# Kernel tuning notes

Hardware: AMD Instinct MI355X
Metric: run time of the kernel (lower is better)

## Reference

```python
import jax, jax.numpy as jnp
import numpy as np

IN_CH, OUT_CH, K, STRIDE, PAD, NUM_POINTS = 16, 32, 3, 1, 1, 3
NUM_INPUTS = IN_CH * K * K  # 144
BATCH, H, W = 8, 32, 32


def setup_inputs() -> dict:
    key = jax.random.key(0)
    k1, k2, k3 = jax.random.split(key, 3)
    x = jax.random.normal(k1, (BATCH, IN_CH, H, W), dtype=jnp.float32)
    # sorted breakpoint positions per (input, output) pair in [-1, 1]
    base = jnp.linspace(-1.0, 1.0, NUM_POINTS, dtype=jnp.float32)
    jitter = 0.2 * (jax.random.uniform(k2, (NUM_INPUTS, OUT_CH, NUM_POINTS), dtype=jnp.float32) - 0.5) / NUM_POINTS
    positions = jnp.sort(base[None, None, :] + jitter, axis=-1)  # (I, O, P), sorted
    values = 0.1 * jax.random.normal(k3, (NUM_INPUTS, OUT_CH, NUM_POINTS), dtype=jnp.float32)
    return {"x": x, "positions": positions, "values": values}


def _gather_pt(table, idx):
    # table: (I, O, P), idx: (N, I, O) -> (N, I, O)
    return jnp.take_along_axis(table[None], idx[..., None], axis=-1)[..., 0]


def _piecewise(patches, positions, values):
    # patches: (N, I); positions/values: (I, O, P)
    P = positions.shape[-1]
    # bucket index: number of breakpoints <= x, clipped to a valid segment
    cmp = patches[:, :, None, None] >= positions[None]       # (N, I, O, P)
    idx = jnp.clip(cmp.sum(axis=-1) - 1, 0, P - 2)           # (N, I, O)
    pl = _gather_pt(positions, idx)
    pr = _gather_pt(positions, idx + 1)
    vl = _gather_pt(values, idx)
    vr = _gather_pt(values, idx + 1)
    t = (patches[:, :, None] - pl) / (pr - pl)               # (N, I, O)
    y = vl + t * (vr - vl)                                   # per-pair piecewise-linear value
    return y.sum(axis=1)                                     # (N, O): sum over input dims


def reference(x, positions, values):
    B, C, Hi, Wi = x.shape
    Ho = (Hi + 2 * PAD - K) // STRIDE + 1
    Wo = (Wi + 2 * PAD - K) // STRIDE + 1
    # im2col / unfold: (B, C*K*K, Ho, Wo) with (c, kh, kw) feature ordering like torch unfold
    patches = jax.lax.conv_general_dilated_patches(
        x, (K, K), (STRIDE, STRIDE), ((PAD, PAD), (PAD, PAD)))
    patches = patches.reshape(B, NUM_INPUTS, Ho * Wo).transpose(0, 2, 1).reshape(-1, NUM_INPUTS)
    out = _piecewise(patches, positions, values)             # (B*Ho*Wo, O)
    out = out.reshape(B, Ho * Wo, OUT_CH).transpose(0, 2, 1)
    return out.reshape(B, OUT_CH, Ho, Wo)
```

## Files before the change

kernel.cpp:

```cpp
#include <hip/hip_runtime.h>

#define IN_CH 16
#define OUT_CH 32
#define NUM_INPUTS 144
#define H_ 32
#define W_ 32
#define TILE_H 8
#define LDS_H 10
#define LDS_W 34
#define CSPLIT 8
#define TAPS (CSPLIT*9)

typedef __attribute__((ext_vector_type(2))) float f32x2;

__global__ void apc_prep(const float* __restrict__ pos,
                         const float* __restrict__ val,
                         float* __restrict__ tabP, float* __restrict__ tabM,
                         float* __restrict__ tabD, float* __restrict__ tabB) {
    int e = blockIdx.x * 256 + threadIdx.x;
    const float* pp = pos + e * 3;
    const float* vv = val + e * 3;
    float p0 = pp[0], p1 = pp[1], p2 = pp[2];
    float v0 = vv[0], v1 = vv[1], v2 = vv[2];
    float m0 = (v1 - v0) / (p1 - p0);
    float m1 = (v2 - v1) / (p2 - p1);
    tabP[e] = p1;
    tabM[e] = m0;
    tabD[e] = m1 - m0;
    tabB[e] = v0 - m0 * p0;
}

__global__ __launch_bounds__(256, 2) void apc_main(
        const float* __restrict__ x,
        const f32x2* __restrict__ tabP, const f32x2* __restrict__ tabM,
        const f32x2* __restrict__ tabD, const f32x2* __restrict__ tabB,
        float* __restrict__ out) {
    __shared__ float lx[CSPLIT * LDS_H * LDS_W];
    __shared__ f32x2 b0s[2];

    int bx  = blockIdx.x;
    int b   = bx >> 2;
    int ho0 = (bx & 3) * TILE_H;
    int pr0 = blockIdx.y * 2;
    int c0  = blockIdx.z * CSPLIT;
    int tid = threadIdx.x;
    int i0  = c0 * 9;

    for (int idx = tid; idx < CSPLIT * LDS_H * LDS_W; idx += 256) {
        int c   = idx / (LDS_H * LDS_W);
        int rem = idx - c * (LDS_H * LDS_W);
        int r   = rem / LDS_W;
        int col = rem - r * LDS_W;
        int gr  = ho0 + r - 1;
        int gc  = col - 1;
        float v = 0.f;
        if ((unsigned)gr < (unsigned)H_ && (unsigned)gc < (unsigned)W_)
            v = x[((b * IN_CH + c0 + c) * H_ + gr) * W_ + gc];
        lx[idx] = v;
    }

    int wave = tid >> 6, lane = tid & 63;
    if (wave < 2) {
        f32x2 s = {0.f, 0.f};
        for (int t = lane; t < TAPS; t += 64)
            s += tabB[(i0 + t) * 16 + pr0 + wave];
        #pragma unroll
        for (int off = 32; off; off >>= 1) {
            s.x += __shfl_down(s.x, off);
            s.y += __shfl_down(s.y, off);
        }
        if (lane == 0) b0s[wave] = s;
    }
    __syncthreads();

    int rl    = tid >> 5;
    int col   = tid & 31;
    int baseA = rl * LDS_W + col;

    f32x2 a0 = {0.f, 0.f}, h0 = {0.f, 0.f};
    f32x2 a1 = {0.f, 0.f}, h1 = {0.f, 0.f};
    const f32x2 zz = {0.f, 0.f};

    #pragma unroll
    for (int c = 0; c < CSPLIT; ++c) {
        #pragma unroll
        for (int kh = 0; kh < 3; ++kh) {
            #pragma unroll
            for (int kw = 0; kw < 3; ++kw) {
                int t  = (c * 3 + kh) * 3 + kw;
                int ti = (i0 + t) * 16;
                float p = lx[c * (LDS_H * LDS_W) + kh * LDS_W + kw + baseA];
                f32x2 pb = {p, p};
                f32x2 P0 = tabP[ti + pr0], P1 = tabP[ti + pr0 + 1];
                f32x2 M0 = tabM[ti + pr0], M1 = tabM[ti + pr0 + 1];
                f32x2 D0 = tabD[ti + pr0], D1 = tabD[ti + pr0 + 1];
                f32x2 r0 = __builtin_elementwise_max(pb - P0, zz);
                f32x2 r1 = __builtin_elementwise_max(pb - P1, zz);
                a0 = __builtin_elementwise_fma(M0, pb, a0);
                a1 = __builtin_elementwise_fma(M1, pb, a1);
                h0 = __builtin_elementwise_fma(D0, r0, h0);
                h1 = __builtin_elementwise_fma(D1, r1, h1);
            }
        }
    }

    a0 += h0 + b0s[0];
    a1 += h1 + b0s[1];

    int ho = ho0 + rl;
    int o0 = pr0 * 2;
    int ob = ((b * OUT_CH + o0) * H_ + ho) * W_ + col;
    atomicAdd(&out[ob            ], a0.x);
    atomicAdd(&out[ob +     H_*W_], a0.y);
    atomicAdd(&out[ob + 2 * H_*W_], a1.x);
    atomicAdd(&out[ob + 3 * H_*W_], a1.y);
}

extern "C" void kernel_launch(void* const* d_in, const int* in_sizes, int n_in,
                              void* d_out, int out_size, void* d_ws, size_t ws_size,
                              hipStream_t stream) {
    const float* x   = (const float*)d_in[0];
    const float* pos = (const float*)d_in[1];
    const float* val = (const float*)d_in[2];

    char* w = (char*)d_ws;
    float* tabP = (float*)(w);
    float* tabM = (float*)(w + 36864);
    float* tabD = (float*)(w + 73728);
    float* tabB = (float*)(w + 110592);

    hipMemsetAsync(d_out, 0, (size_t)out_size * sizeof(float), stream);

    apc_prep<<<18, 256, 0, stream>>>(pos, val, tabP, tabM, tabD, tabB);

    dim3 grid(32, 8, 2);
    apc_main<<<grid, 256, 0, stream>>>(x, (const f32x2*)tabP, (const f32x2*)tabM,
                                       (const f32x2*)tabD, (const f32x2*)tabB,
                                       (float*)d_out);
}
```

Measured before the change: 77.55 us.

## Compute two output rows per thread to reuse table loads across rows

Halves the block size to 128 threads, and each thread now computes two vertically adjacent output rows. It loads four input rows per channel and column tap and shares them across the kh taps, so each table load (P, M, D) is reused for two output pixels and fewer LDS reads are issued per output. Workspace offsets are tightened to match the actual table size (4608 floats each). The cost is more accumulator registers and fewer threads per block, which may reduce latency hiding.

New measurement: 89.29 us. +15.1%, slower.

```diff
diff --git a/kernel.cpp b/kernel.cpp
--- a/kernel.cpp
+++ b/kernel.cpp
@@ -30,7 +30,7 @@
     tabB[e] = v0 - m0 * p0;
 }
 
-__global__ __launch_bounds__(256, 2) void apc_main(
+__global__ __launch_bounds__(128, 1) void apc_main(
         const float* __restrict__ x,
         const f32x2* __restrict__ tabP, const f32x2* __restrict__ tabM,
         const f32x2* __restrict__ tabD, const f32x2* __restrict__ tabB,
@@ -46,7 +46,7 @@
     int tid = threadIdx.x;
     int i0  = c0 * 9;
 
-    for (int idx = tid; idx < CSPLIT * LDS_H * LDS_W; idx += 256) {
+    for (int idx = tid; idx < CSPLIT * LDS_H * LDS_W; idx += 128) {
         int c   = idx / (LDS_H * LDS_W);
         int rem = idx - c * (LDS_H * LDS_W);
         int r   = rem / LDS_W;
@@ -60,7 +60,7 @@
     }
 
     int wave = tid >> 6, lane = tid & 63;
-    if (wave < 2) {
+    {
         f32x2 s = {0.f, 0.f};
         for (int t = lane; t < TAPS; t += 64)
             s += tabB[(i0 + t) * 16 + pr0 + wave];
@@ -73,47 +73,59 @@
     }
     __syncthreads();
 
-    int rl    = tid >> 5;
-    int col   = tid & 31;
-    int baseA = rl * LDS_W + col;
+    int j    = tid >> 5;
+    int col  = tid & 31;
+    int base = (2 * j) * LDS_W + col;
 
-    f32x2 a0 = {0.f, 0.f}, h0 = {0.f, 0.f};
-    f32x2 a1 = {0.f, 0.f}, h1 = {0.f, 0.f};
+    f32x2 aA0 = {0,0}, hA0 = {0,0}, aA1 = {0,0}, hA1 = {0,0};
+    f32x2 aB0 = {0,0}, hB0 = {0,0}, aB1 = {0,0}, hB1 = {0,0};
     const f32x2 zz = {0.f, 0.f};
 
     #pragma unroll
     for (int c = 0; c < CSPLIT; ++c) {
         #pragma unroll
-        for (int kh = 0; kh < 3; ++kh) {
+        for (int kw = 0; kw < 3; ++kw) {
+            float p0 = lx[c * (LDS_H * LDS_W) + base + 0 * LDS_W + kw];
+            float p1 = lx[c * (LDS_H * LDS_W) + base + 1 * LDS_W + kw];
+            float p2 = lx[c * (LDS_H * LDS_W) + base + 2 * LDS_W + kw];
+            float p3 = lx[c * (LDS_H * LDS_W) + base + 3 * LDS_W + kw];
+            float pa[4] = {p0, p1, p2, p3};
             #pragma unroll
-            for (int kw = 0; kw < 3; ++kw) {
-                int t  = (c * 3 + kh) * 3 + kw;
-                int ti = (i0 + t) * 16;
-                float p = lx[c * (LDS_H * LDS_W) + kh * LDS_W + kw + baseA];
-                f32x2 pb = {p, p};
+            for (int kh = 0; kh < 3; ++kh) {
+                int ti = (i0 + (c * 3 + kh) * 3 + kw) * 16;
                 f32x2 P0 = tabP[ti + pr0], P1 = tabP[ti + pr0 + 1];
                 f32x2 M0 = tabM[ti + pr0], M1 = tabM[ti + pr0 + 1];
                 f32x2 D0 = tabD[ti + pr0], D1 = tabD[ti + pr0 + 1];
-                f32x2 r0 = __builtin_elementwise_max(pb - P0, zz);
-                f32x2 r1 = __builtin_elementwise_max(pb - P1, zz);
-                a0 = __builtin_elementwise_fma(M0, pb, a0);
-                a1 = __builtin_elementwise_fma(M1, pb, a1);
-                h0 = __builtin_elementwise_fma(D0, r0, h0);
-                h1 = __builtin_elementwise_fma(D1, r1, h1);
+                f32x2 qA = {pa[kh],     pa[kh]};
+                f32x2 qB = {pa[kh + 1], pa[kh + 1]};
+                aA0 = __builtin_elementwise_fma(M0, qA, aA0);
+                hA0 = __builtin_elementwise_fma(D0, __builtin_elementwise_max(qA - P0, zz), hA0);
+                aA1 = __builtin_elementwise_fma(M1, qA, aA1);
+                hA1 = __builtin_elementwise_fma(D1, __builtin_elementwise_max(qA - P1, zz), hA1);
+                aB0 = __builtin_elementwise_fma(M0, qB, aB0);
+                hB0 = __builtin_elementwise_fma(D0, __builtin_elementwise_max(qB - P0, zz), hB0);
+                aB1 = __builtin_elementwise_fma(M1, qB, aB1);
+                hB1 = __builtin_elementwise_fma(D1, __builtin_elementwise_max(qB - P1, zz), hB1);
             }
         }
     }
 
-    a0 += h0 + b0s[0];
-    a1 += h1 + b0s[1];
+    aA0 += hA0 + b0s[0];  aA1 += hA1 + b0s[1];
+    aB0 += hB0 + b0s[0];  aB1 += hB1 + b0s[1];
 
-    int ho = ho0 + rl;
-    int o0 = pr0 * 2;
-    int ob = ((b * OUT_CH + o0) * H_ + ho) * W_ + col;
-    atomicAdd(&out[ob            ], a0.x);
-    atomicAdd(&out[ob +     H_*W_], a0.y);
-    atomicAdd(&out[ob + 2 * H_*W_], a1.x);
-    atomicAdd(&out[ob + 3 * H_*W_], a1.y);
+    int hoA = ho0 + 2 * j;
+    int o0  = pr0 * 2;
+    int obA = ((b * OUT_CH + o0) * H_ + hoA) * W_ + col;
+    int HW  = H_ * W_;
+    atomicAdd(&out[obA         ], aA0.x);
+    atomicAdd(&out[obA +     HW], aA0.y);
+    atomicAdd(&out[obA + 2 * HW], aA1.x);
+    atomicAdd(&out[obA + 3 * HW], aA1.y);
+    int obB = obA + W_;
+    atomicAdd(&out[obB         ], aB0.x);
+    atomicAdd(&out[obB +     HW], aB0.y);
+    atomicAdd(&out[obB + 2 * HW], aB1.x);
+    atomicAdd(&out[obB + 3 * HW], aB1.y);
 }
 
 extern "C" void kernel_launch(void* const* d_in, const int* in_sizes, int n_in,
@@ -125,16 +137,16 @@
 
     char* w = (char*)d_ws;
     float* tabP = (float*)(w);
-    float* tabM = (float*)(w + 36864);
-    float* tabD = (float*)(w + 73728);
-    float* tabB = (float*)(w + 110592);
+    float* tabM = (float*)(w + 18432);
+    float* tabD = (float*)(w + 36864);
+    float* tabB = (float*)(w + 55296);
 
     hipMemsetAsync(d_out, 0, (size_t)out_size * sizeof(float), stream);
 
     apc_prep<<<18, 256, 0, stream>>>(pos, val, tabP, tabM, tabD, tabB);
 
     dim3 grid(32, 8, 2);
-    apc_main<<<grid, 256, 0, stream>>>(x, (const f32x2*)tabP, (const f32x2*)tabM,
+    apc_main<<<grid, 128, 0, stream>>>(x, (const f32x2*)tabP, (const f32x2*)tabM,
                                        (const f32x2*)tabD, (const f32x2*)tabB,
                                        (float*)d_out);
 }
```
